# Optimization experiments

Hardware: AMD Instinct MI355X
Metric: run time of the kernel (lower is better)

The kernel has to match this reference:

```python
import jax, jax.numpy as jnp
import numpy as np

B, S, D_IN, D_OUT = 4, 4096, 1024, 1024

def setup_inputs() -> dict:
    key = jax.random.key(0)
    kx, kq, kk, kv = jax.random.split(key, 4)
    # torch Linear weights are [out, in]; init scale ~ U(-1/sqrt(in), 1/sqrt(in))
    lim = 1.0 / np.sqrt(D_IN)
    x = jax.random.normal(kx, (B, S, D_IN), dtype=jnp.float32)
    W_query = jax.random.uniform(kq, (D_OUT, D_IN), dtype=jnp.float32, minval=-lim, maxval=lim)
    W_key = jax.random.uniform(kk, (D_OUT, D_IN), dtype=jnp.float32, minval=-lim, maxval=lim)
    W_value = jax.random.uniform(kv, (D_OUT, D_IN), dtype=jnp.float32, minval=-lim, maxval=lim)
    return {"x": x, "W_query": W_query, "W_key": W_key, "W_value": W_value}

def reference(x, W_query, W_key, W_value):
    # Linear: x @ W.T  (torch convention, weight shape [out, in])
    q = jnp.einsum('bsd,od->bso', x, W_query)
    k = jnp.einsum('bsd,od->bso', x, W_key)
    v = jnp.einsum('bsd,od->bso', x, W_value)
    scale = 1.0 / jnp.sqrt(jnp.asarray(k.shape[-1], dtype=x.dtype))
    scores = jnp.einsum('bqo,bko->bqk', q, k) * scale  # [B,S,S]
    weights = jax.nn.softmax(scores, axis=-1)
    return jnp.einsum('bqk,bko->bqo', weights, v)  # [B,S,D_OUT]
```

## Files before the change

kernel.cpp:

```cpp
#include <hip/hip_runtime.h>
#include <cstdint>
#include <cstddef>

typedef __attribute__((ext_vector_type(8))) short short8;
typedef __attribute__((ext_vector_type(4))) float f32x4;

__device__ __forceinline__ unsigned short f2bf(float x) {
  union { float f; unsigned u; } v; v.f = x;
  unsigned r = (v.u + 0x7FFFu + ((v.u >> 16) & 1u)) >> 16;
  return (unsigned short)r;
}
__device__ __forceinline__ float bf2f(unsigned short u) {
  union { unsigned u; float f; } v; v.u = ((unsigned)u) << 16;
  return v.f;
}

#define GLOAD16(g, l)                                                    \
  __builtin_amdgcn_global_load_lds(                                      \
      (const __attribute__((address_space(1))) unsigned int*)(g),        \
      (__attribute__((address_space(3))) unsigned int*)(l), 16, 0, 0)

__global__ __launch_bounds__(256) void cvt_f32_bf16(
    const float* __restrict__ in, unsigned short* __restrict__ out, long n) {
  long i = ((long)blockIdx.x * 256 + threadIdx.x) * 8;
  if (i >= n) return;
  const float4* p = (const float4*)(in + i);
  float4 a = p[0], b = p[1];
  short8 r;
  r[0] = (short)f2bf(a.x); r[1] = (short)f2bf(a.y);
  r[2] = (short)f2bf(a.z); r[3] = (short)f2bf(a.w);
  r[4] = (short)f2bf(b.x); r[5] = (short)f2bf(b.y);
  r[6] = (short)f2bf(b.z); r[7] = (short)f2bf(b.w);
  *(short8*)(out + i) = r;
}

template <bool OUT_BF16>
__global__ __launch_bounds__(512, 2) void gemm_bt256(
    const unsigned short* __restrict__ A, int lda, size_t asb,
    const unsigned short* __restrict__ B, int ldb, size_t bsb,
    void* __restrict__ C, int ldc, size_t csb,
    int nbn, int K, float scale) {
  __shared__ unsigned short As[2][256 * 64];
  __shared__ unsigned short Bs[2][256 * 64];

  A += (size_t)blockIdx.y * asb;
  B += (size_t)blockIdx.y * bsb;
  char* Cb = (char*)C + (size_t)blockIdx.y * csb * (OUT_BF16 ? 2 : 4);

  unsigned bid = blockIdx.x;
  unsigned cpx = gridDim.x >> 3;
  unsigned swz = (bid & 7u) * cpx + (bid >> 3);
  int bm = (int)(swz / (unsigned)nbn);
  int bn = (int)(swz % (unsigned)nbn);
  int m0 = bm * 256, n0 = bn * 256;

  int t512 = threadIdx.x;
  int lane = t512 & 63, wid = t512 >> 6;
  int wm = wid >> 2, wn = wid & 3;
  int l15 = lane & 15, l4 = lane >> 4;

  int srow = t512 >> 3;
  int g = (t512 & 7) ^ ((t512 >> 3) & 7);
  const unsigned short* pa = A + (size_t)(m0 + srow) * lda + g * 8;
  const unsigned short* pb = B + (size_t)(n0 + srow) * ldb + g * 8;

  f32x4 acc[8][4] = {};

  const int NT = K >> 6;

#pragma unroll
  for (int i = 0; i < 4; i++)
    GLOAD16(pa + (size_t)(i * 64) * lda, (char*)As[0] + i * 8192 + t512 * 16);
#pragma unroll
  for (int i = 0; i < 4; i++)
    GLOAD16(pb + (size_t)(i * 64) * ldb, (char*)Bs[0] + i * 8192 + t512 * 16);

  for (int t = 0; t < NT; ++t) {
    int cur = t & 1;
    __builtin_amdgcn_s_barrier();
    if (t + 1 < NT) {
      int k0 = (t + 1) << 6;
#pragma unroll
      for (int i = 0; i < 4; i++)
        GLOAD16(pa + (size_t)(i * 64) * lda + k0,
                (char*)As[cur ^ 1] + i * 8192 + t512 * 16);
#pragma unroll
      for (int i = 0; i < 4; i++)
        GLOAD16(pb + (size_t)(i * 64) * ldb + k0,
                (char*)Bs[cur ^ 1] + i * 8192 + t512 * 16);
      asm volatile("s_waitcnt vmcnt(8)" ::: "memory");
    } else {
      asm volatile("s_waitcnt vmcnt(0)" ::: "memory");
    }
    __builtin_amdgcn_s_barrier();

    const char* Ab = (const char*)As[cur];
    const char* Bb = (const char*)Bs[cur];

    short8 bfv[4][2];
#pragma unroll
    for (int ni = 0; ni < 4; ni++)
#pragma unroll
      for (int ks = 0; ks < 2; ks++) {
        int r = wn * 64 + ni * 16 + l15;
        int c = ((ks << 2) | l4) ^ (r & 7);
        bfv[ni][ks] = *(const short8*)(Bb + r * 128 + c * 16);
      }

#pragma unroll
    for (int q = 0; q < 4; ++q) {
      short8 afv[2][2];
#pragma unroll
      for (int m2 = 0; m2 < 2; m2++)
#pragma unroll
        for (int ks = 0; ks < 2; ks++) {
          int r = wm * 128 + (q * 2 + m2) * 16 + l15;
          int c = ((ks << 2) | l4) ^ (r & 7);
          afv[m2][ks] = *(const short8*)(Ab + r * 128 + c * 16);
        }
      asm volatile("s_waitcnt lgkmcnt(0)" ::: "memory");
      __builtin_amdgcn_sched_barrier(0);
      __builtin_amdgcn_s_setprio(1);
#pragma unroll
      for (int ks = 0; ks < 2; ks++)
#pragma unroll
        for (int m2 = 0; m2 < 2; m2++)
#pragma unroll
          for (int ni = 0; ni < 4; ni++)
            acc[q * 2 + m2][ni] = __builtin_amdgcn_mfma_f32_16x16x32_bf16(
                afv[m2][ks], bfv[ni][ks], acc[q * 2 + m2][ni], 0, 0, 0);
      __builtin_amdgcn_s_setprio(0);
    }
  }

#pragma unroll
  for (int mi = 0; mi < 8; mi++)
#pragma unroll
    for (int ni = 0; ni < 4; ni++)
#pragma unroll
      for (int j = 0; j < 4; j++) {
        int row = m0 + wm * 128 + mi * 16 + l4 * 4 + j;
        int col = n0 + wn * 64 + ni * 16 + l15;
        float val = acc[mi][ni][j] * scale;
        if constexpr (OUT_BF16)
          ((unsigned short*)Cb)[(size_t)row * ldc + col] = f2bf(val);
        else
          ((float*)Cb)[(size_t)row * ldc + col] = val;
      }
}

__global__ __launch_bounds__(256) void softmax_rows(unsigned short* S, int ncols) {
  __shared__ float red[8];
  int row = blockIdx.x;
  unsigned short* p = S + (size_t)row * ncols;
  int t = threadIdx.x;
  int lane = t & 63, wid = t >> 6;

  short8 h0 = ((short8*)p)[t * 2];
  short8 h1 = ((short8*)p)[t * 2 + 1];
  float v[16];
#pragma unroll
  for (int j = 0; j < 8; j++) {
    v[j] = bf2f((unsigned short)h0[j]);
    v[8 + j] = bf2f((unsigned short)h1[j]);
  }
  float m = v[0];
#pragma unroll
  for (int j = 1; j < 16; j++) m = fmaxf(m, v[j]);
#pragma unroll
  for (int off = 1; off < 64; off <<= 1) m = fmaxf(m, __shfl_xor(m, off));
  if (lane == 0) red[wid] = m;
  __syncthreads();
  m = fmaxf(fmaxf(red[0], red[1]), fmaxf(red[2], red[3]));

  float e[16], s = 0.f;
#pragma unroll
  for (int j = 0; j < 16; j++) { e[j] = __expf(v[j] - m); s += e[j]; }
#pragma unroll
  for (int off = 1; off < 64; off <<= 1) s += __shfl_xor(s, off);
  if (lane == 0) red[4 + wid] = s;
  __syncthreads();
  float inv = 1.0f / (red[4] + red[5] + red[6] + red[7]);

  short8 o0, o1;
#pragma unroll
  for (int j = 0; j < 8; j++) {
    o0[j] = (short)f2bf(e[j] * inv);
    o1[j] = (short)f2bf(e[8 + j] * inv);
  }
  ((short8*)p)[t * 2] = o0;
  ((short8*)p)[t * 2 + 1] = o1;
}

extern "C" void kernel_launch(void* const* d_in, const int* in_sizes, int n_in,
                              void* d_out, int out_size, void* d_ws, size_t ws_size,
                              hipStream_t stream) {
  (void)in_sizes; (void)n_in; (void)out_size;
  const float* x  = (const float*)d_in[0];
  const float* Wq = (const float*)d_in[1];
  const float* Wk = (const float*)d_in[2];
  const float* Wv = (const float*)d_in[3];
  float* out = (float*)d_out;

  const int Bn = 4, S = 4096, D = 1024;
  const size_t MS = (size_t)Bn * S;
  const float scale = 0.03125f;

  char* ws = (char*)d_ws;
  unsigned short* QKb = (unsigned short*)ws; ws += MS * 2048 * 2;
  unsigned short* VTb = (unsigned short*)ws; ws += MS * D * 2;
  unsigned short* Sreg = (unsigned short*)ws;
  const size_t s4_bytes = (size_t)Bn * S * S * 2;
  const size_t s1_bytes = (size_t)S * S * 2;
  size_t head = (size_t)(ws - (char*)d_ws);
  bool batched = ws_size >= head + s4_bytes + 6u * 1024 * 1024;
  ws += batched ? s4_bytes : s1_bytes;
  unsigned short* wqkb = (unsigned short*)ws; ws += (size_t)2048 * D * 2;
  unsigned short* wvb  = (unsigned short*)ws;
  unsigned short* xb = Sreg;

  cvt_f32_bf16<<<8192, 256, 0, stream>>>(x, xb, (long)MS * D);
  cvt_f32_bf16<<<512, 256, 0, stream>>>(Wq, wqkb, (long)D * D);
  cvt_f32_bf16<<<512, 256, 0, stream>>>(Wk, wqkb + (size_t)D * D, (long)D * D);
  cvt_f32_bf16<<<512, 256, 0, stream>>>(Wv, wvb, (long)D * D);

  gemm_bt256<true><<<dim3(512, 1), 512, 0, stream>>>(
      xb, D, 0, wqkb, D, 0, QKb, 2048, 0, 8, D, 1.0f);
  gemm_bt256<true><<<dim3(256, 1), 512, 0, stream>>>(
      wvb, D, 0, xb, D, 0, VTb, (int)MS, 0, 64, D, 1.0f);

  if (batched) {
    gemm_bt256<true><<<dim3(256, Bn), 512, 0, stream>>>(
        QKb, 2048, (size_t)S * 2048,
        QKb + 1024, 2048, (size_t)S * 2048,
        Sreg, S, (size_t)S * S, 16, D, scale);
    softmax_rows<<<(int)MS, 256, 0, stream>>>(Sreg, S);
    gemm_bt256<false><<<dim3(64, Bn), 512, 0, stream>>>(
        Sreg, S, (size_t)S * S,
        VTb, (int)MS, (size_t)S,
        out, D, (size_t)S * D, 4, S, 1.0f);
  } else {
    for (int b = 0; b < Bn; b++) {
      const unsigned short* Qx = QKb + (size_t)b * S * 2048;
      const unsigned short* Kx = Qx + 1024;
      gemm_bt256<true><<<dim3(256, 1), 512, 0, stream>>>(
          Qx, 2048, 0, Kx, 2048, 0, Sreg, S, 0, 16, D, scale);
      softmax_rows<<<S, 256, 0, stream>>>(Sreg, S);
      gemm_bt256<false><<<dim3(64, 1), 512, 0, stream>>>(
          Sreg, S, 0, VTb + (size_t)b * S, (int)MS, 0,
          out + (size_t)b * S * D, D, 0, 4, S, 1.0f);
    }
  }
}
```

Baseline: 464.5 us.

## Replace double-buffered K=64 tiles with a 4-stage K=32 prefetch pipeline

The bf16 GEMM main loop changes from two 64-wide K buffers to four 32-wide K buffers, with three stages of global-to-LDS loads kept in flight. vmcnt waits are adjusted for how many stages remain, and the LDS XOR swizzle is reworked for 64-byte rows. The aim is to hide more global-memory latency behind MFMA work at the same LDS footprint. The cost is twice as many loop iterations and barriers, less MFMA work per barrier, and possible new LDS bank conflicts from the narrower row layout.

```diff
diff --git a/kernel.cpp b/kernel.cpp
--- a/kernel.cpp
+++ b/kernel.cpp
@@ -40,8 +40,8 @@
     const unsigned short* __restrict__ B, int ldb, size_t bsb,
     void* __restrict__ C, int ldc, size_t csb,
     int nbn, int K, float scale) {
-  __shared__ unsigned short As[2][256 * 64];
-  __shared__ unsigned short Bs[2][256 * 64];
+  __shared__ unsigned short As[4][256 * 32];
+  __shared__ unsigned short Bs[4][256 * 32];
 
   A += (size_t)blockIdx.y * asb;
   B += (size_t)blockIdx.y * bsb;
@@ -59,79 +59,75 @@
   int wm = wid >> 2, wn = wid & 3;
   int l15 = lane & 15, l4 = lane >> 4;
 
-  int srow = t512 >> 3;
-  int g = (t512 & 7) ^ ((t512 >> 3) & 7);
+  int srow = t512 >> 2;
+  int g = (t512 & 3) ^ ((t512 >> 3) & 3);
   const unsigned short* pa = A + (size_t)(m0 + srow) * lda + g * 8;
   const unsigned short* pb = B + (size_t)(n0 + srow) * ldb + g * 8;
 
   f32x4 acc[8][4] = {};
 
-  const int NT = K >> 6;
-
-#pragma unroll
-  for (int i = 0; i < 4; i++)
-    GLOAD16(pa + (size_t)(i * 64) * lda, (char*)As[0] + i * 8192 + t512 * 16);
-#pragma unroll
-  for (int i = 0; i < 4; i++)
-    GLOAD16(pb + (size_t)(i * 64) * ldb, (char*)Bs[0] + i * 8192 + t512 * 16);
-
-  for (int t = 0; t < NT; ++t) {
-    int cur = t & 1;
+  const int NT = K >> 5;
+
+#define STAGE(jj)                                                         \
+  do {                                                                    \
+    int _b = (jj) & 3;                                                    \
+    int _k0 = (jj) << 5;                                                  \
+    GLOAD16(pa + _k0, (char*)As[_b] + t512 * 16);                         \
+    GLOAD16(pa + (size_t)128 * lda + _k0,                                 \
+            (char*)As[_b] + 8192 + t512 * 16);                            \
+    GLOAD16(pb + _k0, (char*)Bs[_b] + t512 * 16);                         \
+    GLOAD16(pb + (size_t)128 * ldb + _k0,                                 \
+            (char*)Bs[_b] + 8192 + t512 * 16);                            \
+  } while (0)
+
+  STAGE(0);
+  STAGE(1);
+  STAGE(2);
+
+  for (int j = 0; j < NT; ++j) {
     __builtin_amdgcn_s_barrier();
-    if (t + 1 < NT) {
-      int k0 = (t + 1) << 6;
-#pragma unroll
-      for (int i = 0; i < 4; i++)
-        GLOAD16(pa + (size_t)(i * 64) * lda + k0,
-                (char*)As[cur ^ 1] + i * 8192 + t512 * 16);
-#pragma unroll
-      for (int i = 0; i < 4; i++)
-        GLOAD16(pb + (size_t)(i * 64) * ldb + k0,
-                (char*)Bs[cur ^ 1] + i * 8192 + t512 * 16);
+    int rem = NT - 1 - j;
+    if (rem >= 3) {
+      STAGE(j + 3);
+      asm volatile("s_waitcnt vmcnt(12)" ::: "memory");
+    } else if (rem == 2) {
       asm volatile("s_waitcnt vmcnt(8)" ::: "memory");
+    } else if (rem == 1) {
+      asm volatile("s_waitcnt vmcnt(4)" ::: "memory");
     } else {
       asm volatile("s_waitcnt vmcnt(0)" ::: "memory");
     }
     __builtin_amdgcn_s_barrier();
 
-    const char* Ab = (const char*)As[cur];
-    const char* Bb = (const char*)Bs[cur];
-
-    short8 bfv[4][2];
-#pragma unroll
-    for (int ni = 0; ni < 4; ni++)
-#pragma unroll
-      for (int ks = 0; ks < 2; ks++) {
-        int r = wn * 64 + ni * 16 + l15;
-        int c = ((ks << 2) | l4) ^ (r & 7);
-        bfv[ni][ks] = *(const short8*)(Bb + r * 128 + c * 16);
-      }
-
-#pragma unroll
-    for (int q = 0; q < 4; ++q) {
-      short8 afv[2][2];
-#pragma unroll
-      for (int m2 = 0; m2 < 2; m2++)
-#pragma unroll
-        for (int ks = 0; ks < 2; ks++) {
-          int r = wm * 128 + (q * 2 + m2) * 16 + l15;
-          int c = ((ks << 2) | l4) ^ (r & 7);
-          afv[m2][ks] = *(const short8*)(Ab + r * 128 + c * 16);
-        }
-      asm volatile("s_waitcnt lgkmcnt(0)" ::: "memory");
-      __builtin_amdgcn_sched_barrier(0);
-      __builtin_amdgcn_s_setprio(1);
-#pragma unroll
-      for (int ks = 0; ks < 2; ks++)
-#pragma unroll
-        for (int m2 = 0; m2 < 2; m2++)
-#pragma unroll
-          for (int ni = 0; ni < 4; ni++)
-            acc[q * 2 + m2][ni] = __builtin_amdgcn_mfma_f32_16x16x32_bf16(
-                afv[m2][ks], bfv[ni][ks], acc[q * 2 + m2][ni], 0, 0, 0);
-      __builtin_amdgcn_s_setprio(0);
-    }
-  }
+    const char* Ab = (const char*)As[j & 3];
+    const char* Bb = (const char*)Bs[j & 3];
+
+    short8 bfv[4];
+#pragma unroll
+    for (int ni = 0; ni < 4; ni++) {
+      int r = wn * 64 + ni * 16 + l15;
+      int slot = l4 ^ ((r >> 1) & 3);
+      bfv[ni] = *(const short8*)(Bb + r * 64 + slot * 16);
+    }
+    short8 afv[8];
+#pragma unroll
+    for (int mi = 0; mi < 8; mi++) {
+      int r = wm * 128 + mi * 16 + l15;
+      int slot = l4 ^ ((r >> 1) & 3);
+      afv[mi] = *(const short8*)(Ab + r * 64 + slot * 16);
+    }
+    asm volatile("s_waitcnt lgkmcnt(0)" ::: "memory");
+    __builtin_amdgcn_sched_barrier(0);
+    __builtin_amdgcn_s_setprio(1);
+#pragma unroll
+    for (int mi = 0; mi < 8; mi++)
+#pragma unroll
+      for (int ni = 0; ni < 4; ni++)
+        acc[mi][ni] = __builtin_amdgcn_mfma_f32_16x16x32_bf16(
+            afv[mi], bfv[ni], acc[mi][ni], 0, 0, 0);
+    __builtin_amdgcn_s_setprio(0);
+  }
+#undef STAGE
 
 #pragma unroll
   for (int mi = 0; mi < 8; mi++)
```

New measurement: 516.2 us. +11.1%, slower.
